# Kernel tuning notes

Hardware: AMD Instinct MI355X
Metric: run time of the kernel (lower is better)

## Reference

```python
import jax, jax.numpy as jnp
import numpy as np
import math
from jax import lax

HID, H, K = 1024, 8, 4
D = HID // H
B, T = 2, 2048
CLAMP_MAX = 0.999995
LN_EPS = 1e-5

def _logit(x):
    x = min(max(x, 1e-06), 1 - 1e-06)
    return math.log(x / (1 - x))

def setup_inputs() -> dict:
    key = jax.random.key(0)
    ks = jax.random.split(key, 8)
    def xavier(k, fan_in, fan_out):
        s = math.sqrt(2.0 / (fan_in + fan_out))
        return jax.random.normal(k, (fan_in, fan_out), jnp.float32) * s
    x = jax.random.normal(ks[0], (B, T, HID), jnp.float32)
    mask = jnp.ones((B, T), jnp.float32)
    Wq = xavier(ks[1], HID, HID)
    Wk = xavier(ks[2], HID, HID)
    Wv = xavier(ks[3], HID, HID)
    Wb = xavier(ks[4], HID, H)
    bb = jnp.full((H,), _logit(0.99), jnp.float32)
    Wm = xavier(ks[5], HID, H * K)
    bm = jnp.zeros((H * K,), jnp.float32)
    Wo = xavier(ks[6], HID, HID)
    bo = jnp.zeros((HID,), jnp.float32)
    base = np.array([_logit(math.exp(-1.0 / t)) for t in [16.0, 64.0, 256.0, 1024.0]], np.float32)
    base_logit = jnp.asarray(np.tile(base[None, :], (H, 1)))  # (H, K)
    ln_g = jnp.ones((HID,), jnp.float32)
    ln_b = jnp.zeros((HID,), jnp.float32)
    return dict(x=x, mask=mask, Wq=Wq, Wk=Wk, Wv=Wv, Wb=Wb, bb=bb, Wm=Wm, bm=bm,
                Wo=Wo, bo=bo, base_logit=base_logit, ln_g=ln_g, ln_b=ln_b)

def _delta_scan(q, k, v, beta, mix, mask, base_logit):
    # q,k,v: (B,T,H,D); beta: (B,T,H); mix: (B,T,H,K); mask: (B,T)
    b, t = q.shape[0], q.shape[1]
    base_r = jax.nn.sigmoid(base_logit)  # (H,K)
    state0 = jnp.zeros((b, H, K, D, D), jnp.float32)

    def step(state, inp):
        q_t, k_t, v_t, b_t, mix_t, m_t = inp
        valid = (m_t > 0)[:, None, None, None, None]            # (B,1,1,1,1)
        r_eff = jnp.clip(b_t[:, :, None] * base_r[None], 0.0, CLAMP_MAX)  # (B,H,K)
        outer = jnp.einsum('bhd,bhe->bhde', k_t, v_t)[:, :, None]          # (B,H,1,D,D)
        new_state = jnp.where(valid, state * r_eff[..., None, None] + outer, state)
        o_scales = jnp.einsum('bhd,bhkde->bhke', q_t, new_state)           # (B,H,K,D)
        w = jax.nn.softmax(mix_t, axis=-1)                                  # (B,H,K)
        o_t = jnp.sum(w[..., None] * o_scales, axis=2)                      # (B,H,D)
        o_t = o_t * (m_t > 0)[:, None, None].astype(o_t.dtype)
        return new_state, o_t

    xs = (jnp.moveaxis(q, 1, 0), jnp.moveaxis(k, 1, 0), jnp.moveaxis(v, 1, 0),
          jnp.moveaxis(beta, 1, 0), jnp.moveaxis(mix, 1, 0), jnp.moveaxis(mask, 1, 0))
    _, outs = lax.scan(step, state0, xs)       # (T,B,H,D)
    return jnp.moveaxis(outs, 0, 1)            # (B,T,H,D)

def reference(x, mask, Wq, Wk, Wv, Wb, bb, Wm, bm, Wo, bo, base_logit, ln_g, ln_b):
    b, t, _ = x.shape
    def elu1(z):
        return jax.nn.elu(z) + 1.0
    q = elu1((x @ Wq).reshape(b, t, H, D))
    k = elu1((x @ Wk).reshape(b, t, H, D))
    v = (x @ Wv).reshape(b, t, H, D)
    beta = jax.nn.sigmoid(x @ Wb + bb)               # (B,T,H)
    mix = (x @ Wm + bm).reshape(b, t, H, K)          # (B,T,H,K)
    head_out = _delta_scan(q, k, v, beta, mix, mask, base_logit)  # (B,T,H,D)
    out = head_out.reshape(b, t, HID) @ Wo + bo
    y = x + out                                       # residual (dropout in eval mode)
    mu = jnp.mean(y, axis=-1, keepdims=True)
    var = jnp.mean((y - mu) ** 2, axis=-1, keepdims=True)
    return (y - mu) * lax.rsqrt(var + LN_EPS) * ln_g + ln_b
```

## Files before the change

kernel.cpp:

```cpp
#include <hip/hip_runtime.h>
#include <hip/hip_bf16.h>
#include <math.h>

#define TSEQ 2048
#define NHID 1024

typedef float f32x4 __attribute__((ext_vector_type(4)));
typedef __bf16 bf16x8 __attribute__((ext_vector_type(8)));

static __device__ __forceinline__ unsigned short f2bf(float f) {
  unsigned u = __float_as_uint(f);
  u += 0x7fffu + ((u >> 16) & 1u);
  return (unsigned short)(u >> 16);
}
static __device__ __forceinline__ float bf2f(unsigned short h) {
  return __uint_as_float(((unsigned)h) << 16);
}

#define GLDS16(g, l) __builtin_amdgcn_global_load_lds( \
    (const __attribute__((address_space(1))) unsigned int*)(g), \
    (__attribute__((address_space(3))) unsigned int*)(l), 16, 0, 0)

__global__ __launch_bounds__(256) void transpose_all_kernel(
    const float* __restrict__ Wq, const float* __restrict__ Wk,
    const float* __restrict__ Wv, const float* __restrict__ Wo,
    const float* __restrict__ Wb, const float* __restrict__ Wm,
    unsigned short* __restrict__ Wqkvt, unsigned short* __restrict__ Wto,
    float* __restrict__ Wtf) {
  int m = blockIdx.z;
  int tx = threadIdx.x, ty = threadIdx.y;
  if (m == 4) {
    int blk = blockIdx.y * 32 + blockIdx.x;
    if (blk >= 160) return;
    int id = blk * 256 + ty * 32 + tx;
    int o = id >> 10, i = id & 1023;
    Wtf[id] = (o < 8) ? Wb[i * 8 + o] : Wm[i * 32 + (o - 8)];
    return;
  }
  __shared__ float tile[32][33];
  const float* W;
  unsigned short* Wt;
  if (m == 0)      { W = Wq; Wt = Wqkvt; }
  else if (m == 1) { W = Wk; Wt = Wqkvt + 1024 * 1024; }
  else if (m == 2) { W = Wv; Wt = Wqkvt + 2 * 1024 * 1024; }
  else             { W = Wo; Wt = Wto; }
  int bx = blockIdx.x * 32;
  int by = blockIdx.y * 32;
#pragma unroll
  for (int i = 0; i < 32; i += 8)
    tile[ty + i][tx] = W[(size_t)(by + ty + i) * NHID + bx + tx];
  __syncthreads();
#pragma unroll
  for (int i = 0; i < 32; i += 8)
    Wt[(size_t)(bx + ty + i) * NHID + by + tx] = f2bf(tile[tx][ty + i]);
}

template <int MODE>
__global__ __launch_bounds__(256) void gemm_pipe_kernel(
    const unsigned short* __restrict__ A, const unsigned short* __restrict__ Bt,
    unsigned short* __restrict__ Oq, unsigned short* __restrict__ Ok,
    unsigned short* __restrict__ Ov, unsigned short* __restrict__ Pbase) {
  __shared__ __align__(16) unsigned short As[3 * 4096];
  __shared__ __align__(16) unsigned short Bs[3 * 4096];
  const int tid = threadIdx.x;
  const int lane = tid & 63;
  const int wave = tid >> 6;
  const int wr = wave >> 1, wc = wave & 1;
  const int rowBase = blockIdx.y * 128;
  const int colBase = blockIdx.x * 128;
  const int NT = (MODE == 0) ? 32 : 16;
  const int kOff = (MODE == 0) ? 0 : blockIdx.z * 512;

  const int c0 = wave * 128 + lane;
  const int c1 = c0 + 64;
  const int r0 = c0 >> 2, kc0 = (c0 & 3) ^ ((r0 >> 1) & 3);
  const int r1 = c1 >> 2, kc1 = (c1 & 3) ^ ((r1 >> 1) & 3);
  const unsigned short* gA0 = A + (size_t)(rowBase + r0) * 1024 + kOff + kc0 * 8;
  const unsigned short* gA1 = A + (size_t)(rowBase + r1) * 1024 + kOff + kc1 * 8;
  const unsigned short* gB0 = Bt + (size_t)(colBase + r0) * 1024 + kOff + kc0 * 8;
  const unsigned short* gB1 = Bt + (size_t)(colBase + r1) * 1024 + kOff + kc1 * 8;
  const int wofs = wave * 1024;

  const int kq = lane >> 4;
  const int r16 = lane & 15;

  f32x4 acc[4][4] = {};

#define STAGE(buf, k0)                                       \
  do {                                                       \
    GLDS16(gA0 + (k0), &As[(buf) * 4096 + wofs]);            \
    GLDS16(gA1 + (k0), &As[(buf) * 4096 + wofs + 512]);      \
    GLDS16(gB0 + (k0), &Bs[(buf) * 4096 + wofs]);            \
    GLDS16(gB1 + (k0), &Bs[(buf) * 4096 + wofs + 512]);      \
  } while (0)

  STAGE(0, 0);
  STAGE(1, 32);
  int cur = 0, stg = 2;
  for (int t = 0; t < NT; ++t) {
    if (t < NT - 2) {
      STAGE(stg, (t + 2) * 32);
      asm volatile("s_waitcnt vmcnt(8)" ::: "memory");
    } else if (t == NT - 2) {
      asm volatile("s_waitcnt vmcnt(4)" ::: "memory");
    } else {
      asm volatile("s_waitcnt vmcnt(0)" ::: "memory");
    }
    __builtin_amdgcn_s_barrier();
    asm volatile("" ::: "memory");
    const unsigned short* Ac = &As[cur * 4096];
    const unsigned short* Bc = &Bs[cur * 4096];
    bf16x8 af[4], bfr[4];
#pragma unroll
    for (int m = 0; m < 4; ++m) {
      int row = wr * 64 + m * 16 + r16;
      af[m] = *(const bf16x8*)(Ac + row * 32 + (kq ^ ((row >> 1) & 3)) * 8);
      int colr = wc * 64 + m * 16 + r16;
      bfr[m] = *(const bf16x8*)(Bc + colr * 32 + (kq ^ ((colr >> 1) & 3)) * 8);
    }
#pragma unroll
    for (int m = 0; m < 4; ++m)
#pragma unroll
      for (int n = 0; n < 4; ++n)
        acc[m][n] = __builtin_amdgcn_mfma_f32_16x16x32_bf16(af[m], bfr[n], acc[m][n], 0, 0, 0);
    asm volatile("" ::: "memory");
    __builtin_amdgcn_s_barrier();
    asm volatile("" ::: "memory");
    cur = (cur == 2) ? 0 : cur + 1;
    stg = (stg == 2) ? 0 : stg + 1;
  }
#undef STAGE

  const int r4 = (lane >> 4) * 4;
  if (MODE == 1) {
    unsigned short* P = Pbase + (size_t)blockIdx.z * 4096 * 1024;
#pragma unroll
    for (int m = 0; m < 4; ++m)
#pragma unroll
      for (int n = 0; n < 4; ++n) {
        int col = colBase + wc * 64 + n * 16 + r16;
#pragma unroll
        for (int j = 0; j < 4; ++j) {
          int row = rowBase + wr * 64 + m * 16 + r4 + j;
          P[(size_t)row * 1024 + col] = f2bf(acc[m][n][j]);
        }
      }
  } else {
    unsigned short* outp;
    int cb;
    bool elu;
    if (colBase < 1024)      { outp = Oq; cb = colBase;        elu = true;  }
    else if (colBase < 2048) { outp = Ok; cb = colBase - 1024; elu = true;  }
    else                     { outp = Ov; cb = colBase - 2048; elu = false; }
#pragma unroll
    for (int m = 0; m < 4; ++m)
#pragma unroll
      for (int n = 0; n < 4; ++n) {
        int col = cb + wc * 64 + n * 16 + r16;
#pragma unroll
        for (int j = 0; j < 4; ++j) {
          int row = rowBase + wr * 64 + m * 16 + r4 + j;
          float v = acc[m][n][j];
          if (elu) v = (v > 0.f) ? (v + 1.f) : expf(v);
          outp[(size_t)row * 1024 + col] = f2bf(v);
        }
      }
  }
}

__global__ __launch_bounds__(256) void rw8_kernel(const float* __restrict__ x,
    const float* __restrict__ Wt, const float* __restrict__ bb,
    const float* __restrict__ bm, const float* __restrict__ base_logit,
    float* __restrict__ R, float* __restrict__ Wsm,
    unsigned short* __restrict__ Xb) {
  __shared__ float xs[8][1024];
  __shared__ float outs[8][40];
  int row0 = blockIdx.x * 8;
  int tid = threadIdx.x;
#pragma unroll
  for (int r = 0; r < 8; ++r) {
    float4 xv = *(const float4*)(x + (size_t)(row0 + r) * 1024 + tid * 4);
    *(float4*)(&xs[r][tid * 4]) = xv;
    ushort4 xo;
    xo.x = f2bf(xv.x); xo.y = f2bf(xv.y); xo.z = f2bf(xv.z); xo.w = f2bf(xv.w);
    *(ushort4*)(Xb + (size_t)(row0 + r) * 1024 + tid * 4) = xo;
  }
  __syncthreads();
  int wave = tid >> 6, lane = tid & 63;
  for (int o = wave; o < 40; o += 4) {
    const float* wr = Wt + o * 1024;
    float w[16];
#pragma unroll
    for (int it = 0; it < 16; ++it) w[it] = wr[it * 64 + lane];
#pragma unroll
    for (int r = 0; r < 8; ++r) {
      float sum = 0.f;
#pragma unroll
      for (int it = 0; it < 16; ++it) sum += xs[r][it * 64 + lane] * w[it];
#pragma unroll
      for (int off = 32; off > 0; off >>= 1) sum += __shfl_down(sum, off);
      if (lane == 0) outs[r][o] = sum;
    }
  }
  __syncthreads();
  {
    int r = tid >> 5, j = tid & 31;
    int row = row0 + r;
    int h = j >> 2;
    float beta = 1.f / (1.f + expf(-(outs[r][h] + bb[h])));
    float br = 1.f / (1.f + expf(-base_logit[j]));
    float rr = fminf(fmaxf(beta * br, 0.f), 0.999995f);
    float mval = outs[r][8 + j] + bm[j];
    float mx = fmaxf(mval, __shfl_xor(mval, 1));
    mx = fmaxf(mx, __shfl_xor(mx, 2));
    float ex = expf(mval - mx);
    float ssum = ex + __shfl_xor(ex, 1);
    ssum += __shfl_xor(ssum, 2);
    R[(size_t)row * 32 + j] = rr;
    Wsm[(size_t)row * 32 + j] = ex / ssum;
  }
}

__global__ __launch_bounds__(256) void decay2_kernel(const float* __restrict__ R,
    const float* __restrict__ Wsm, const float* __restrict__ mask,
    float* __restrict__ WA, float* __restrict__ IA, float* __restrict__ DU,
    float* __restrict__ AC) {
  int wave = threadIdx.x >> 6, lane = threadIdx.x & 63;
  int id = blockIdx.x * 4 + wave;
  int c = id & 15, k = (id >> 4) & 3, bh = id >> 6;
  int b = bh >> 3, h = bh & 7;
  int row0 = b * TSEQ + c * 128 + 2 * lane;
  float m0 = mask[row0], m1 = mask[row0 + 1];
  size_t i0 = (size_t)row0 * 32 + h * 4 + k;
  float rr0 = (m0 > 0.f) ? R[i0] : 1.f;
  float rr1 = (m1 > 0.f) ? R[i0 + 32] : 1.f;
  float incl = rr0 * rr1;
#pragma unroll
  for (int off = 1; off < 64; off <<= 1) {
    float o = __shfl_up(incl, off);
    if (lane >= off) incl *= o;
  }
  float excl = __shfl_up(incl, 1);
  if (lane == 0) excl = 1.f;
  float a0 = fmaxf(excl * rr0, 1e-25f);
  float a1 = fmaxf(a0 * rr1, 1e-25f);
  float aC = __shfl(a1, 63);
  if (lane == 63) AC[(bh * 16 + c) * 4 + k] = a1;
  bool v0 = m0 > 0.f, v1 = m1 > 0.f;
  float w0 = Wsm[i0], w1 = Wsm[i0 + 32];
  int dub = ((bh * 16 + c) * 4 + k) * 128 + 2 * lane;
  WA[i0] = v0 ? w0 * a0 : 0.f;
  WA[i0 + 32] = v1 ? w1 * a1 : 0.f;
  IA[i0] = v0 ? 1.f / a0 : 0.f;
  IA[i0 + 32] = v1 ? 1.f / a1 : 0.f;
  DU[dub] = v0 ? aC / a0 : 0.f;
  DU[dub + 1] = v1 ? aC / a1 : 0.f;
}

#define KV_SLOT(j, d) (((j) ^ ((d) & 7) ^ (((d) >> 3) & 7)) << 4)

__global__ __launch_bounds__(512) void chunkA_kernel(
    const unsigned short* __restrict__ Qb, const unsigned short* __restrict__ Kb,
    const unsigned short* __restrict__ Vb,
    const float* __restrict__ WA, const float* __restrict__ IA,
    const float* __restrict__ DU,
    unsigned short* __restrict__ Olb, unsigned short* __restrict__ UT) {
  __shared__ __align__(16) char KTl[32768];
  __shared__ __align__(16) char VTl[32768];
  __shared__ __align__(16) char Pl[32768];
  __shared__ __align__(16) float WAl[128][4];
  __shared__ __align__(16) float IAl[128][4];
  __shared__ float DUl[4][128];

  int wg = blockIdx.x;
  int bh = wg >> 4, c = wg & 15;
  int b = bh >> 3, h = bh & 7;
  int t0 = c * 128;
  int tid = threadIdx.x;
  int lane = tid & 63, wave = tid >> 6;
  int wbase = wave * 16;
  int l15 = lane & 15, lq = lane >> 4;

  const size_t qkvbase = ((size_t)b * TSEQ + t0) * 1024 + h * 128;

  for (int it = 0; it < 2; ++it) {
    int ci = tid + it * 512;
    int t = (ci >> 4) * 2, s = ci & 15;
    bf16x8 k0 = *(const bf16x8*)(Kb + qkvbase + (size_t)t * 1024 + s * 8);
    bf16x8 k1 = *(const bf16x8*)(Kb + qkvbase + (size_t)(t + 1) * 1024 + s * 8);
    bf16x8 v0 = *(const bf16x8*)(Vb + qkvbase + (size_t)t * 1024 + s * 8);
    bf16x8 v1 = *(const bf16x8*)(Vb + qkvbase + (size_t)(t + 1) * 1024 + s * 8);
    const unsigned short* k0u = (const unsigned short*)&k0;
    const unsigned short* k1u = (const unsigned short*)&k1;
    const unsigned short* v0u = (const unsigned short*)&v0;
    const unsigned short* v1u = (const unsigned short*)&v1;
#pragma unroll
    for (int e = 0; e < 8; ++e) {
      int d = s * 8 + e;
      int off = d * 256 + (((t >> 3) ^ (d & 7) ^ ((d >> 3) & 7)) << 4) + (t & 7) * 2;
      *(unsigned int*)(KTl + off) = (unsigned)k0u[e] | ((unsigned)k1u[e] << 16);
      *(unsigned int*)(VTl + off) = (unsigned)v0u[e] | ((unsigned)v1u[e] << 16);
    }
  }
  {
    int t = tid >> 2, k = tid & 3;
    size_t idx = ((size_t)b * TSEQ + t0 + t) * 32 + h * 4 + k;
    WAl[t][k] = WA[idx];
    IAl[t][k] = IA[idx];
    int k2 = tid >> 7, j = tid & 127;
    DUl[k2][j] = DU[((bh * 16 + c) * 4 + k2) * 128 + j];
  }
  __syncthreads();

  bf16x8 qf[4];
#pragma unroll
  for (int ds = 0; ds < 4; ++ds)
    qf[ds] = *(const bf16x8*)(Qb + qkvbase + (size_t)(wbase + l15) * 1024 + ds * 32 + lq * 8);
  f32x4 accP[8];
#pragma unroll
  for (int jf = 0; jf < 8; ++jf) {
    f32x4 a = {};
#pragma unroll
    for (int ds = 0; ds < 4; ++ds) {
      bf16x8 kfrag = *(const bf16x8*)(Kb + qkvbase + (size_t)(jf * 16 + l15) * 1024 + ds * 32 + lq * 8);
      a = __builtin_amdgcn_mfma_f32_16x16x32_bf16(qf[ds], kfrag, a, 0, 0, 0);
    }
    accP[jf] = a;
  }

  float4 wa4[4];
#pragma unroll
  for (int jj = 0; jj < 4; ++jj)
    wa4[jj] = *(const float4*)&WAl[wbase + lq * 4 + jj][0];
#pragma unroll
  for (int jf = 0; jf < 8; ++jf) {
    float4 ia4 = *(const float4*)&IAl[jf * 16 + l15][0];
#pragma unroll
    for (int jj = 0; jj < 4; ++jj) {
      int tl = wbase + lq * 4 + jj;
      int jl = jf * 16 + l15;
      float m = 0.f;
      if (jl <= tl)
        m = wa4[jj].x * ia4.x + wa4[jj].y * ia4.y + wa4[jj].z * ia4.z + wa4[jj].w * ia4.w;
      float pv = accP[jf][jj] * m;
      int off = tl * 256 + (((jl >> 3) ^ (tl & 7)) << 4) + (jl & 7) * 2;
      *(unsigned short*)(Pl + off) = f2bf(pv);
    }
  }

  bf16x8 pf[4];
#pragma unroll
  for (int js = 0; js < 4; ++js) {
    int tl = wbase + l15;
    int slot = js * 4 + lq;
    pf[js] = *(const bf16x8*)(Pl + tl * 256 + ((slot ^ (tl & 7)) << 4));
  }
#pragma unroll
  for (int dvf = 0; dvf < 8; ++dvf) {
    f32x4 a = {};
    int dv = dvf * 16 + l15;
#pragma unroll
    for (int js = 0; js < 4; ++js) {
      int slot = js * 4 + lq;
      bf16x8 vfrag = *(const bf16x8*)(VTl + dv * 256 + KV_SLOT(slot, dv));
      a = __builtin_amdgcn_mfma_f32_16x16x32_bf16(pf[js], vfrag, a, 0, 0, 0);
    }
#pragma unroll
    for (int jj = 0; jj < 4; ++jj) {
      int tl = wbase + lq * 4 + jj;
      Olb[((size_t)b * TSEQ + t0 + tl) * 1024 + h * 128 + dv] = f2bf(a[jj]);
    }
  }

  if (c < 15) {
#pragma unroll 1
    for (int k = 0; k < 4; ++k) {
      f32x4 accU[8] = {};
#pragma unroll 1
      for (int js = 0; js < 4; ++js) {
        int dvr = wbase + l15;
        int slot = js * 4 + lq;
        bf16x8 af = *(const bf16x8*)(VTl + dvr * 256 + KV_SLOT(slot, dvr));
        int j0 = js * 32 + lq * 8;
        bf16x8 afs;
#pragma unroll
        for (int e = 0; e < 8; ++e)
          afs[e] = (__bf16)((float)af[e] * DUl[k][j0 + e]);
#pragma unroll
        for (int dkf = 0; dkf < 8; ++dkf) {
          int dk = dkf * 16 + l15;
          bf16x8 kf = *(const bf16x8*)(KTl + dk * 256 + KV_SLOT(slot, dk));
          accU[dkf] = __builtin_amdgcn_mfma_f32_16x16x32_bf16(afs, kf, accU[dkf], 0, 0, 0);
        }
      }
      size_t ub = (((size_t)bh * 16 + c) * 4 + k) * 16384;
#pragma unroll
      for (int dkf = 0; dkf < 8; ++dkf) {
        int dk = dkf * 16 + l15;
#pragma unroll
        for (int jj = 0; jj < 4; ++jj) {
          int dvr = wbase + lq * 4 + jj;
          UT[ub + (size_t)dvr * 128 + dk] = f2bf(accU[dkf][jj]);
        }
      }
    }
  }
}

__global__ __launch_bounds__(256) void chainB_kernel(const unsigned short* __restrict__ UT,
    const float* __restrict__ AC, unsigned short* __restrict__ S0T) {
  int id = blockIdx.x * 256 + threadIdx.x;
  int dk4 = id & 31;
  int dv = (id >> 5) & 127;
  int k = (id >> 12) & 3;
  int bh = id >> 14;
  size_t elem = (size_t)dv * 128 + dk4 * 4;
  float S0 = 0.f, S1 = 0.f, S2 = 0.f, S3 = 0.f;
#pragma unroll 1
  for (int c = 0; c < 15; ++c) {
    size_t ub = (((size_t)bh * 16 + c) * 4 + k) * 16384 + elem;
    ushort4 u = *(const ushort4*)(UT + ub);
    float aC = AC[(bh * 16 + c) * 4 + k];
    S0 = aC * S0 + bf2f(u.x);
    S1 = aC * S1 + bf2f(u.y);
    S2 = aC * S2 + bf2f(u.z);
    S3 = aC * S3 + bf2f(u.w);
    size_t sb = (((size_t)bh * 16 + (c + 1)) * 4 + k) * 16384 + elem;
    ushort4 o;
    o.x = f2bf(S0); o.y = f2bf(S1); o.z = f2bf(S2); o.w = f2bf(S3);
    *(ushort4*)(S0T + sb) = o;
  }
}

__global__ __launch_bounds__(512) void chunkC_kernel(const unsigned short* __restrict__ Qb,
    const unsigned short* __restrict__ S0T, const float* __restrict__ WA,
    const unsigned short* __restrict__ Olb, unsigned short* __restrict__ Ob) {
  __shared__ __align__(16) char Sl[32768];
  int wg = blockIdx.x;
  int bh = wg >> 4, c = wg & 15;
  int b = bh >> 3, h = bh & 7;
  int t0 = c * 128;
  int tid = threadIdx.x, lane = tid & 63, wave = tid >> 6;
  int l15 = lane & 15, lq = lane >> 4, wbase = wave * 16;
  size_t qbase = ((size_t)b * TSEQ + t0) * 1024 + h * 128;

  f32x4 accO[8] = {};
  if (c > 0) {
    int tl = wbase + l15;
    size_t so[4];
#pragma unroll
    for (int it = 0; it < 4; ++it) {
      int ci = tid + it * 512;
      int dv = ci >> 4, s = ci & 15;
      so[it] = (size_t)dv * 128 + (size_t)(s ^ (dv & 7)) * 8;
    }
#pragma unroll 1
    for (int k = 0; k < 4; ++k) {
      __syncthreads();
      size_t sb = (((size_t)bh * 16 + c) * 4 + k) * 16384;
      GLDS16(S0T + sb + so[0], (unsigned short*)(Sl + wave * 1024));
      GLDS16(S0T + sb + so[1], (unsigned short*)(Sl + 8192 + wave * 1024));
      GLDS16(S0T + sb + so[2], (unsigned short*)(Sl + 16384 + wave * 1024));
      GLDS16(S0T + sb + so[3], (unsigned short*)(Sl + 24576 + wave * 1024));
      asm volatile("s_waitcnt vmcnt(0)" ::: "memory");
      __syncthreads();
      float sc = WA[((size_t)b * TSEQ + t0 + tl) * 32 + h * 4 + k];
#pragma unroll 1
      for (int ds = 0; ds < 4; ++ds) {
        bf16x8 qf = *(const bf16x8*)(Qb + qbase + (size_t)tl * 1024 + ds * 32 + lq * 8);
        bf16x8 qs;
#pragma unroll
        for (int e = 0; e < 8; ++e) qs[e] = (__bf16)((float)qf[e] * sc);
#pragma unroll
        for (int dvf = 0; dvf < 8; ++dvf) {
          int dv = dvf * 16 + l15;
          int slot = ds * 4 + lq;
          bf16x8 sf = *(const bf16x8*)(Sl + dv * 256 + ((slot ^ (dv & 7)) << 4));
          accO[dvf] = __builtin_amdgcn_mfma_f32_16x16x32_bf16(qs, sf, accO[dvf], 0, 0, 0);
        }
      }
    }
  }
#pragma unroll
  for (int dvf = 0; dvf < 8; ++dvf) {
    int dv = dvf * 16 + l15;
#pragma unroll
    for (int jj = 0; jj < 4; ++jj) {
      int tl = wbase + lq * 4 + jj;
      size_t off = ((size_t)b * TSEQ + t0 + tl) * 1024 + h * 128 + dv;
      Ob[off] = f2bf(accO[dvf][jj] + bf2f(Olb[off]));
    }
  }
}

__global__ __launch_bounds__(256) void ln_kernel(const unsigned short* __restrict__ Pbase,
    const float* __restrict__ bo, const float* __restrict__ xres,
    const float* __restrict__ g, const float* __restrict__ bta,
    float* __restrict__ out) {
  int row = blockIdx.x;
  int tid = threadIdx.x;
  int lane = tid & 63, wave = tid >> 6;
  __shared__ float red[8];
  size_t base = (size_t)row * 1024 + tid * 4;
  const size_t PS = (size_t)4096 * 1024;
  ushort4 a = *(const ushort4*)(Pbase + base);
  ushort4 b2 = *(const ushort4*)(Pbase + PS + base);
  float4 xv = *(const float4*)(xres + base);
  float4 bv = *(const float4*)(bo + tid * 4);
  float4 v;
  v.x = bf2f(a.x) + bf2f(b2.x) + bv.x + xv.x;
  v.y = bf2f(a.y) + bf2f(b2.y) + bv.y + xv.y;
  v.z = bf2f(a.z) + bf2f(b2.z) + bv.z + xv.z;
  v.w = bf2f(a.w) + bf2f(b2.w) + bv.w + xv.w;
  float sum = v.x + v.y + v.z + v.w;
#pragma unroll
  for (int off = 32; off > 0; off >>= 1) sum += __shfl_down(sum, off);
  if (lane == 0) red[wave] = sum;
  __syncthreads();
  float mu = (red[0] + red[1] + red[2] + red[3]) * (1.f / 1024.f);
  float4 d;
  d.x = v.x - mu; d.y = v.y - mu; d.z = v.z - mu; d.w = v.w - mu;
  float sq = d.x * d.x + d.y * d.y + d.z * d.z + d.w * d.w;
#pragma unroll
  for (int off = 32; off > 0; off >>= 1) sq += __shfl_down(sq, off);
  __syncthreads();
  if (lane == 0) red[4 + wave] = sq;
  __syncthreads();
  float var = (red[4] + red[5] + red[6] + red[7]) * (1.f / 1024.f);
  float inv = rsqrtf(var + 1e-5f);
  float4 gg = *(const float4*)(g + tid * 4);
  float4 bb4 = *(const float4*)(bta + tid * 4);
  float4 o;
  o.x = d.x * inv * gg.x + bb4.x;
  o.y = d.y * inv * gg.y + bb4.y;
  o.z = d.z * inv * gg.z + bb4.z;
  o.w = d.w * inv * gg.w + bb4.w;
  *(float4*)(out + (size_t)row * 1024 + tid * 4) = o;
}

extern "C" void kernel_launch(void* const* d_in, const int* in_sizes, int n_in,
                              void* d_out, int out_size, void* d_ws, size_t ws_size,
                              hipStream_t stream) {
  const float* x    = (const float*)d_in[0];
  const float* mask = (const float*)d_in[1];
  const float* Wq   = (const float*)d_in[2];
  const float* Wk   = (const float*)d_in[3];
  const float* Wv   = (const float*)d_in[4];
  const float* Wb   = (const float*)d_in[5];
  const float* bb   = (const float*)d_in[6];
  const float* Wm   = (const float*)d_in[7];
  const float* bm   = (const float*)d_in[8];
  const float* Wo   = (const float*)d_in[9];
  const float* bo   = (const float*)d_in[10];
  const float* base_logit = (const float*)d_in[11];
  const float* ln_g = (const float*)d_in[12];
  const float* ln_b = (const float*)d_in[13];

  char* ws = (char*)d_ws;
  const size_t MB = 1024u * 1024u;
  unsigned short* Xb    = (unsigned short*)(ws + 0);
  unsigned short* Wqkvt = (unsigned short*)(ws + 8 * MB);
  unsigned short* Wto   = (unsigned short*)(ws + 14 * MB);
  float* Rf  = (float*)(ws + 16 * MB);
  float* Wsf = (float*)(ws + 16 * MB + 512 * 1024);
  float* WAf = (float*)(ws + 17 * MB);
  float* IAf = (float*)(ws + 17 * MB + 512 * 1024);
  float* DUf = (float*)(ws + 18 * MB);
  float* ACf = (float*)(ws + 18 * MB + 512 * 1024);
  float* Wtf = (float*)(ws + 18 * MB + 768 * 1024);
  unsigned short* Qb  = (unsigned short*)(ws + 19 * MB);
  unsigned short* Kb  = (unsigned short*)(ws + 27 * MB);
  unsigned short* Vb  = (unsigned short*)(ws + 35 * MB);
  unsigned short* Olb = (unsigned short*)(ws + 43 * MB);
  unsigned short* Ob  = (unsigned short*)(ws + 51 * MB);
  unsigned short* UTb = (unsigned short*)(ws + 59 * MB);
  unsigned short* S0T = (unsigned short*)(ws + 91 * MB);
  unsigned short* Pp = (unsigned short*)(ws + 59 * MB);
  if (ws_size < 131 * MB) return;

  dim3 tb(32, 8), tg(32, 32, 5);
  transpose_all_kernel<<<tg, tb, 0, stream>>>(Wq, Wk, Wv, Wo, Wb, Wm, Wqkvt, Wto, Wtf);

  rw8_kernel<<<512, 256, 0, stream>>>(x, Wtf, bb, bm, base_logit, Rf, Wsf, Xb);
  decay2_kernel<<<256, 256, 0, stream>>>(Rf, Wsf, mask, WAf, IAf, DUf, ACf);

  dim3 gqkv(24, 32);
  gemm_pipe_kernel<0><<<gqkv, 256, 0, stream>>>(Xb, Wqkvt, Qb, Kb, Vb, nullptr);

  chunkA_kernel<<<256, 512, 0, stream>>>(Qb, Kb, Vb, WAf, IAf, DUf, Olb, UTb);
  chainB_kernel<<<1024, 256, 0, stream>>>(UTb, ACf, S0T);
  chunkC_kernel<<<256, 512, 0, stream>>>(Qb, S0T, WAf, Olb, Ob);

  dim3 gwo(8, 32, 2);
  gemm_pipe_kernel<1><<<gwo, 256, 0, stream>>>(Ob, Wto, nullptr, nullptr, nullptr, Pp);

  ln_kernel<<<4096, 256, 0, stream>>>(Pp, bo, x, ln_g, ln_b, (float*)d_out);
}
```

Baseline: 163.0 us.

## Store intra-chunk outputs and chunk states in fragment-native layout; double-buffer state loads

The chunk kernel now writes its intra-chunk output and per-chunk state updates in the MFMA accumulator order (wave/lane-contiguous) rather than row-major, so its stores are coalesced. The chain and combine kernels are adjusted to read that permuted layout, with the LDS staging offsets remapped to match. chunkC also double-buffers the per-k state tile in LDS, prefetching the next k while computing the current one, and hoists the Q fragment loads out of the k loop. This trades simpler indexing and one extra 32KB LDS buffer for fewer uncoalesced global accesses and overlapped load latency.

```diff
diff --git a/kernel.cpp b/kernel.cpp
--- a/kernel.cpp
+++ b/kernel.cpp
@@ -355,6 +355,7 @@
     int slot = js * 4 + lq;
     pf[js] = *(const bf16x8*)(Pl + tl * 256 + ((slot ^ (tl & 7)) << 4));
   }
+  size_t olb = (size_t)wg * 16384 + wave * 2048 + lane;
 #pragma unroll
   for (int dvf = 0; dvf < 8; ++dvf) {
     f32x4 a = {};
@@ -366,10 +367,8 @@
       a = __builtin_amdgcn_mfma_f32_16x16x32_bf16(pf[js], vfrag, a, 0, 0, 0);
     }
 #pragma unroll
-    for (int jj = 0; jj < 4; ++jj) {
-      int tl = wbase + lq * 4 + jj;
-      Olb[((size_t)b * TSEQ + t0 + tl) * 1024 + h * 128 + dv] = f2bf(a[jj]);
-    }
+    for (int jj = 0; jj < 4; ++jj)
+      Olb[olb + (dvf * 4 + jj) * 64] = f2bf(a[jj]);
   }
 
   if (c < 15) {
@@ -393,16 +392,12 @@
           accU[dkf] = __builtin_amdgcn_mfma_f32_16x16x32_bf16(afs, kf, accU[dkf], 0, 0, 0);
         }
       }
-      size_t ub = (((size_t)bh * 16 + c) * 4 + k) * 16384;
-#pragma unroll
-      for (int dkf = 0; dkf < 8; ++dkf) {
-        int dk = dkf * 16 + l15;
-#pragma unroll
-        for (int jj = 0; jj < 4; ++jj) {
-          int dvr = wbase + lq * 4 + jj;
-          UT[ub + (size_t)dvr * 128 + dk] = f2bf(accU[dkf][jj]);
-        }
-      }
+      size_t ub = (((size_t)bh * 16 + c) * 4 + k) * 16384 + wave * 2048 + lane;
+#pragma unroll
+      for (int dkf = 0; dkf < 8; ++dkf)
+#pragma unroll
+        for (int jj = 0; jj < 4; ++jj)
+          UT[ub + (dkf * 4 + jj) * 64] = f2bf(accU[dkf][jj]);
     }
   }
 }
@@ -410,11 +405,10 @@
 __global__ __launch_bounds__(256) void chainB_kernel(const unsigned short* __restrict__ UT,
     const float* __restrict__ AC, unsigned short* __restrict__ S0T) {
   int id = blockIdx.x * 256 + threadIdx.x;
-  int dk4 = id & 31;
-  int dv = (id >> 5) & 127;
+  int q = id & 4095;
   int k = (id >> 12) & 3;
   int bh = id >> 14;
-  size_t elem = (size_t)dv * 128 + dk4 * 4;
+  size_t elem = (size_t)q * 4;
   float S0 = 0.f, S1 = 0.f, S2 = 0.f, S3 = 0.f;
 #pragma unroll 1
   for (int c = 0; c < 15; ++c) {
@@ -435,7 +429,7 @@
 __global__ __launch_bounds__(512) void chunkC_kernel(const unsigned short* __restrict__ Qb,
     const unsigned short* __restrict__ S0T, const float* __restrict__ WA,
     const unsigned short* __restrict__ Olb, unsigned short* __restrict__ Ob) {
-  __shared__ __align__(16) char Sl[32768];
+  __shared__ __align__(16) char Sl[2][32768];
   int wg = blockIdx.x;
   int bh = wg >> 4, c = wg & 15;
   int b = bh >> 3, h = bh & 7;
@@ -451,36 +445,57 @@
 #pragma unroll
     for (int it = 0; it < 4; ++it) {
       int ci = tid + it * 512;
-      int dv = ci >> 4, s = ci & 15;
-      so[it] = (size_t)dv * 128 + (size_t)(s ^ (dv & 7)) * 8;
-    }
+      int dv = ci >> 4, p = ci & 15;
+      int s = p ^ (dv & 7);
+      so[it] = (size_t)(dv >> 4) * 2048 + (size_t)((s >> 1) * 4 + (dv & 3)) * 64
+             + (size_t)((dv >> 2) & 3) * 16 + (size_t)(s & 1) * 8;
+    }
+    bf16x8 qf[4];
+#pragma unroll
+    for (int ds = 0; ds < 4; ++ds)
+      qf[ds] = *(const bf16x8*)(Qb + qbase + (size_t)tl * 1024 + ds * 32 + lq * 8);
+
+#define STAGE_S(buf, kk) do { \
+      size_t sb = (((size_t)bh * 16 + c) * 4 + (kk)) * 16384; \
+      GLDS16(S0T + sb + so[0], (unsigned short*)(Sl[buf] + wave * 1024)); \
+      GLDS16(S0T + sb + so[1], (unsigned short*)(Sl[buf] + 8192 + wave * 1024)); \
+      GLDS16(S0T + sb + so[2], (unsigned short*)(Sl[buf] + 16384 + wave * 1024)); \
+      GLDS16(S0T + sb + so[3], (unsigned short*)(Sl[buf] + 24576 + wave * 1024)); \
+    } while (0)
+
+    STAGE_S(0, 0);
 #pragma unroll 1
     for (int k = 0; k < 4; ++k) {
-      __syncthreads();
-      size_t sb = (((size_t)bh * 16 + c) * 4 + k) * 16384;
-      GLDS16(S0T + sb + so[0], (unsigned short*)(Sl + wave * 1024));
-      GLDS16(S0T + sb + so[1], (unsigned short*)(Sl + 8192 + wave * 1024));
-      GLDS16(S0T + sb + so[2], (unsigned short*)(Sl + 16384 + wave * 1024));
-      GLDS16(S0T + sb + so[3], (unsigned short*)(Sl + 24576 + wave * 1024));
-      asm volatile("s_waitcnt vmcnt(0)" ::: "memory");
-      __syncthreads();
+      if (k < 3) {
+        STAGE_S((k + 1) & 1, k + 1);
+        asm volatile("s_waitcnt vmcnt(4)" ::: "memory");
+      } else {
+        asm volatile("s_waitcnt vmcnt(0)" ::: "memory");
+      }
+      __builtin_amdgcn_s_barrier();
+      asm volatile("" ::: "memory");
+      const char* Sc = Sl[k & 1];
       float sc = WA[((size_t)b * TSEQ + t0 + tl) * 32 + h * 4 + k];
 #pragma unroll 1
       for (int ds = 0; ds < 4; ++ds) {
-        bf16x8 qf = *(const bf16x8*)(Qb + qbase + (size_t)tl * 1024 + ds * 32 + lq * 8);
         bf16x8 qs;
 #pragma unroll
-        for (int e = 0; e < 8; ++e) qs[e] = (__bf16)((float)qf[e] * sc);
+        for (int e = 0; e < 8; ++e) qs[e] = (__bf16)((float)qf[ds][e] * sc);
 #pragma unroll
         for (int dvf = 0; dvf < 8; ++dvf) {
           int dv = dvf * 16 + l15;
           int slot = ds * 4 + lq;
-          bf16x8 sf = *(const bf16x8*)(Sl + dv * 256 + ((slot ^ (dv & 7)) << 4));
+          bf16x8 sf = *(const bf16x8*)(Sc + dv * 256 + ((slot ^ (dv & 7)) << 4));
           accO[dvf] = __builtin_amdgcn_mfma_f32_16x16x32_bf16(qs, sf, accO[dvf], 0, 0, 0);
         }
       }
-    }
-  }
+      asm volatile("" ::: "memory");
+      __builtin_amdgcn_s_barrier();
+      asm volatile("" ::: "memory");
+    }
+#undef STAGE_S
+  }
+  size_t olb = (size_t)wg * 16384 + wave * 2048 + lane;
 #pragma unroll
   for (int dvf = 0; dvf < 8; ++dvf) {
     int dv = dvf * 16 + l15;
@@ -488,7 +503,8 @@
     for (int jj = 0; jj < 4; ++jj) {
       int tl = wbase + lq * 4 + jj;
       size_t off = ((size_t)b * TSEQ + t0 + tl) * 1024 + h * 128 + dv;
-      Ob[off] = f2bf(accO[dvf][jj] + bf2f(Olb[off]));
+      float ol = bf2f(Olb[olb + (dvf * 4 + jj) * 64]);
+      Ob[off] = f2bf(accO[dvf][jj] + ol);
     }
   }
 }
```

New measurement: 209.5 us. +28.5%, slower.
